# Kernel tuning notes

Measured on AMD Instinct MI355X. Metric: run time of the kernel, lower is better.

Reference implementation:

```python
import jax, jax.numpy as jnp
import numpy as np

EMBED = 1024
HEADS = 16
HEAD_DIM = EMBED // HEADS


def setup_inputs() -> dict:
    key = jax.random.key(0)
    ks = jax.random.split(key, 9)
    s = 1.0 / np.sqrt(EMBED)
    inp = {
        "x": jax.random.normal(ks[0], (2, 2048, EMBED), dtype=jnp.float32),
        "wq": jax.random.uniform(ks[1], (EMBED, EMBED), jnp.float32, -s, s),
        "bq": jax.random.uniform(ks[2], (EMBED,), jnp.float32, -s, s),
        "wk": jax.random.uniform(ks[3], (EMBED, EMBED), jnp.float32, -s, s),
        "bk": jax.random.uniform(ks[4], (EMBED,), jnp.float32, -s, s),
        "wv": jax.random.uniform(ks[5], (EMBED, EMBED), jnp.float32, -s, s),
        "bv": jax.random.uniform(ks[6], (EMBED,), jnp.float32, -s, s),
        "wo": jax.random.uniform(ks[7], (EMBED, EMBED), jnp.float32, -s, s),
        "bo": jax.random.uniform(ks[8], (EMBED,), jnp.float32, -s, s),
    }
    return inp


def reference(x, wq, bq, wk, bk, wv, bv, wo, bo):
    B, S, E = x.shape
    H, D = HEADS, HEAD_DIM
    # projections (torch Linear: y = x @ W.T + b; here weights stored as [E, E] applied as x @ W.T)
    q = (x @ wq.T + bq).reshape(B, S, H, D).transpose(0, 2, 1, 3)  # [B,H,S,D]
    k = (x @ wk.T + bk).reshape(B, S, H, D).transpose(0, 2, 1, 3)
    v = (x @ wv.T + bv).reshape(B, S, H, D).transpose(0, 2, 1, 3)
    scores = jnp.einsum("bhqd,bhkd->bhqk", q, k) / jnp.sqrt(jnp.asarray(D, x.dtype))
    attn = jax.nn.softmax(scores, axis=-1)  # dropout is identity in eval / p=0
    ctx = jnp.einsum("bhqk,bhkd->bhqd", attn, v)
    ctx = ctx.transpose(0, 2, 1, 3).reshape(B, S, E)
    return ctx @ wo.T + bo
```

## Files before the change

### kernel.cpp

```cpp
#include <hip/hip_runtime.h>
#include <hip/hip_bf16.h>

#define EMBED 1024
#define HEADS 16
#define HDIM  64
#define BATCH 2
#define SEQ   2048
#define MTOT  (BATCH*SEQ)

typedef __attribute__((ext_vector_type(8))) short bf16x8;
typedef __attribute__((ext_vector_type(4))) short bf16x4;
typedef __attribute__((ext_vector_type(4))) float f32x4;
typedef __attribute__((ext_vector_type(8))) unsigned short u16x8;
typedef __attribute__((ext_vector_type(2))) unsigned u32x2;
typedef __attribute__((ext_vector_type(4))) unsigned u32x4;

__device__ __forceinline__ unsigned pack2(float lo, float hi) {
    __hip_bfloat162 h = __float22bfloat162_rn(make_float2(lo, hi));
    unsigned u;
    __builtin_memcpy(&u, &h, sizeof(u));
    return u;
}
__device__ __forceinline__ unsigned short f2bf(float f) {
    __hip_bfloat16 h = __float2bfloat16(f);
    unsigned short u;
    __builtin_memcpy(&u, &h, sizeof(u));
    return u;
}

__device__ __forceinline__ void glds16(const void* g, void* l) {
    __builtin_amdgcn_global_load_lds(
        (const __attribute__((address_space(1))) void*)g,
        (__attribute__((address_space(3))) void*)l, 16, 0, 0);
}

__global__ __launch_bounds__(256) void preconvert(
    const float* __restrict__ x,
    const float* __restrict__ wq, const float* __restrict__ wk,
    const float* __restrict__ wv, const float* __restrict__ wo,
    unsigned short* __restrict__ xb,
    unsigned short* __restrict__ wqb, unsigned short* __restrict__ wkb,
    unsigned short* __restrict__ wvb, unsigned short* __restrict__ wob)
{
    const int NX = (MTOT * EMBED) / 4;
    const int NW = (EMBED * EMBED) / 4;
    int idx = blockIdx.x * 256 + threadIdx.x;
    const float* src;
    unsigned short* dst;
    int off;
    if (idx < NX) {
        src = x; dst = xb; off = idx;
    } else {
        int r = idx - NX;
        int w = r / NW;
        off = r - w * NW;
        src = (w == 0) ? wq : (w == 1) ? wk : (w == 2) ? wv : wo;
        dst = (w == 0) ? wqb : (w == 1) ? wkb : (w == 2) ? wvb : wob;
    }
    float4 v = ((const float4*)src)[off];
    u32x2 o;
    o[0] = pack2(v.x, v.y);
    o[1] = pack2(v.z, v.w);
    *(u32x2*)(dst + (size_t)off * 4) = o;
}

__global__ __launch_bounds__(256, 2) void qkv_proj(
    const unsigned short* __restrict__ xb,
    const unsigned short* __restrict__ wqb, const float* __restrict__ bq,
    const unsigned short* __restrict__ wkb, const float* __restrict__ bk,
    const unsigned short* __restrict__ wvb, const float* __restrict__ bv,
    unsigned short* __restrict__ qo,
    unsigned short* __restrict__ ko,
    unsigned short* __restrict__ vto)
{
    const int which = blockIdx.z;
    const unsigned short* __restrict__ w =
        (which == 0) ? wqb : (which == 1) ? wkb : wvb;
    const float* __restrict__ bias = (which == 0) ? bq : (which == 1) ? bk : bv;
    const float kscale = (which == 1) ? 0.18033688f : 1.0f;

    const int m0 = blockIdx.x * 128;
    const int n0 = blockIdx.y * 128;

    __shared__ __align__(16) unsigned short a_lds[128 * 32];
    __shared__ __align__(16) unsigned short b_lds[128 * 32];

    const int tid  = threadIdx.x;
    const int lane = tid & 63;
    const int wid  = tid >> 6;
    const int wr   = wid >> 1, wc = wid & 1;
    const int lq   = lane & 15;
    const int lg   = lane >> 4;

    f32x4 acc[4][4] = {};

    const int srow  = wid * 32 + (lane >> 2);
    const int scol8 = (lane & 3) * 8;
    const unsigned short* ap0 = xb + (size_t)(m0 + srow)      * EMBED + scol8;
    const unsigned short* ap1 = xb + (size_t)(m0 + srow + 16) * EMBED + scol8;
    const unsigned short* bp0 = w  + (size_t)(n0 + srow)      * EMBED + scol8;
    const unsigned short* bp1 = w  + (size_t)(n0 + srow + 16) * EMBED + scol8;
    unsigned short* la0 = a_lds + wid * 1024;
    unsigned short* la1 = a_lds + wid * 1024 + 512;
    unsigned short* lb0 = b_lds + wid * 1024;
    unsigned short* lb1 = b_lds + wid * 1024 + 512;

    for (int k0 = 0; k0 < EMBED; k0 += 32) {
        glds16(ap0 + k0, la0);
        glds16(ap1 + k0, la1);
        glds16(bp0 + k0, lb0);
        glds16(bp1 + k0, lb1);
        __syncthreads();
        bf16x8 af[4], bfr[4];
        #pragma unroll
        for (int i = 0; i < 4; ++i)
            af[i] = *(const bf16x8*)&a_lds[(wr*64 + i*16 + lq) * 32 + lg*8];
        #pragma unroll
        for (int j = 0; j < 4; ++j)
            bfr[j] = *(const bf16x8*)&b_lds[(wc*64 + j*16 + lq) * 32 + lg*8];
        #pragma unroll
        for (int i = 0; i < 4; ++i)
            #pragma unroll
            for (int j = 0; j < 4; ++j)
                acc[i][j] = __builtin_amdgcn_mfma_f32_16x16x32_bf16(af[i], bfr[j], acc[i][j], 0, 0, 0);
        __syncthreads();
    }

    #pragma unroll
    for (int j = 0; j < 4; ++j) {
        const int nn = n0 + wc*64 + j*16 + lq;
        const float bsv = bias[nn];
        const int h = nn >> 6, d = nn & (HDIM-1);
        #pragma unroll
        for (int i = 0; i < 4; ++i) {
            const int mmb = m0 + wr*64 + i*16 + lg*4;
            const int b = mmb >> 11;
            const int s = mmb & (SEQ-1);
            const size_t bh = (size_t)(b*HEADS + h);
            if (which == 2) {
                u32x2 ov;
                ov[0] = pack2(acc[i][j][0] + bsv, acc[i][j][1] + bsv);
                ov[1] = pack2(acc[i][j][2] + bsv, acc[i][j][3] + bsv);
                *(u32x2*)&vto[(bh*HDIM + d)*SEQ + s] = ov;
            } else {
                unsigned short* o = (which == 0) ? qo : ko;
                #pragma unroll
                for (int r = 0; r < 4; ++r)
                    o[(bh*SEQ + (s + r))*HDIM + d] = f2bf((acc[i][j][r] + bsv) * kscale);
            }
        }
    }
}

__global__ __launch_bounds__(256, 2) void attn(
    const unsigned short* __restrict__ q,
    const unsigned short* __restrict__ k,
    const unsigned short* __restrict__ vt,
    unsigned short* __restrict__ ctx)
{
    __shared__ __align__(16) unsigned char sm[2 * 16384];

    const int bid   = blockIdx.x;
    const int xcd   = bid & 7;
    const int local = bid >> 3;
    const int bh    = xcd * 4 + (local >> 4);
    const int q0    = (local & 15) * 128;
    const int b     = bh >> 4;
    const int h     = bh & (HEADS - 1);
    const int tid   = threadIdx.x;
    const int wv    = tid >> 6;
    const int lane  = tid & 63;
    const int lq = lane & 15, lg = lane >> 4;

    const unsigned short* qb = q  + (size_t)bh * SEQ * HDIM;
    const unsigned short* kb = k  + (size_t)bh * SEQ * HDIM;
    const unsigned short* vb = vt + (size_t)bh * HDIM * SEQ;

    const int lg16 = lg * 16;
    const int Sp = (((lq & 3) | (((lq >> 2) & 1) << 2)) << 4);
    const int Tp = (((lq & 3) | (((lq >> 3) & 1) << 2)) << 4);
    const int kreadA = (8*(lq >> 2) + (lq & 3)) * 128 + (lg16 ^ Sp);
    const int kreadB = kreadA ^ 64;
    const int vreadA = lq * 128 + (lg16 ^ Tp);
    const int vreadB = vreadA ^ 64;

    const int wrow = tid >> 3;
    const int c8   = tid & 7;
    const int wS   = (((wrow & 3) | (((wrow >> 3) & 1) << 2)) << 4);
    const int woff = wrow * 128 + ((c8 * 16) ^ wS);

    const int scol = c8 * 8;
    const unsigned short* kp = kb + (size_t)wrow * HDIM + scol;
    const unsigned short* vp = vb + (size_t)wrow * SEQ + scol;

    bf16x8 qf[2][2];
    #pragma unroll
    for (int t = 0; t < 2; ++t)
        #pragma unroll
        for (int hh = 0; hh < 2; ++hh)
            qf[t][hh] = *(const bf16x8*)(qb + (size_t)(q0 + wv*32 + t*16 + lq) * HDIM + hh*32 + lg*8);

    u16x8 ones_u;
    #pragma unroll
    for (int e = 0; e < 8; ++e) ones_u[e] = 0x3F80;
    const bf16x8 ones = __builtin_bit_cast(bf16x8, ones_u);

    f32x4 o[2][4] = {};
    f32x4 acc_l[2] = {};

    u16x8 kr0, kr1, vr0, vr1;

#define LOADT() do {                                                           \
    kr0 = *(const u16x8*)(kp);                                                 \
    kr1 = *(const u16x8*)(kp + 32*HDIM);                                       \
    vr0 = *(const u16x8*)(vp);                                                 \
    vr1 = *(const u16x8*)(vp + 32*SEQ);                                        \
} while (0)

#define WRITET(BF) do {                                                        \
    unsigned char* smb = sm + (BF)*16384;                                      \
    *(u16x8*)(smb +         woff) = kr0;                                       \
    *(u16x8*)(smb +  4096 + woff) = kr1;                                       \
    *(u16x8*)(smb +  8192 + woff) = vr0;                                       \
    *(u16x8*)(smb + 12288 + woff) = vr1;                                       \
} while (0)

#define COMPUTE(BF) do {                                                       \
    const unsigned char* smb = sm + (BF)*16384;                                \
    f32x4 s_[2][4];                                                            \
    _Pragma("unroll")                                                          \
    for (int sub = 0; sub < 4; ++sub) {                                        \
        const int sadd = (sub & 1) * 512 + (sub >> 1) * 4096;                  \
        bf16x8 k0 = *(const bf16x8*)(smb + sadd + kreadA);                     \
        bf16x8 k1 = *(const bf16x8*)(smb + sadd + kreadB);                     \
        _Pragma("unroll")                                                      \
        for (int t = 0; t < 2; ++t) {                                          \
            f32x4 z = {};                                                      \
            z = __builtin_amdgcn_mfma_f32_16x16x32_bf16(k0, qf[t][0], z, 0, 0, 0); \
            z = __builtin_amdgcn_mfma_f32_16x16x32_bf16(k1, qf[t][1], z, 0, 0, 0); \
            s_[t][sub] = z;                                                    \
        }                                                                      \
    }                                                                          \
    bf16x8 pb[2][2];                                                           \
    _Pragma("unroll")                                                          \
    for (int t = 0; t < 2; ++t) {                                              \
        u32x4 pw0, pw1;                                                        \
        _Pragma("unroll")                                                      \
        for (int sub = 0; sub < 4; ++sub) {                                    \
            f32x4 pv;                                                          \
            _Pragma("unroll")                                                  \
            for (int r = 0; r < 4; ++r) pv[r] = exp2f(s_[t][sub][r]);          \
            unsigned d0 = pack2(pv[0], pv[1]);                                 \
            unsigned d1 = pack2(pv[2], pv[3]);                                 \
            if (sub == 0)      { pw0[0] = d0; pw0[1] = d1; }                   \
            else if (sub == 1) { pw0[2] = d0; pw0[3] = d1; }                   \
            else if (sub == 2) { pw1[0] = d0; pw1[1] = d1; }                   \
            else               { pw1[2] = d0; pw1[3] = d1; }                   \
        }                                                                      \
        pb[t][0] = __builtin_bit_cast(bf16x8, pw0);                            \
        pb[t][1] = __builtin_bit_cast(bf16x8, pw1);                            \
        acc_l[t] = __builtin_amdgcn_mfma_f32_16x16x32_bf16(ones, pb[t][0], acc_l[t], 0, 0, 0); \
        acc_l[t] = __builtin_amdgcn_mfma_f32_16x16x32_bf16(ones, pb[t][1], acc_l[t], 0, 0, 0); \
    }                                                                          \
    _Pragma("unroll")                                                          \
    for (int i = 0; i < 4; ++i) {                                              \
        bf16x8 va  = *(const bf16x8*)(smb + 8192 + i*2048 + vreadA);           \
        bf16x8 vbq = *(const bf16x8*)(smb + 8192 + i*2048 + vreadB);           \
        _Pragma("unroll")                                                      \
        for (int t = 0; t < 2; ++t) {                                          \
            o[t][i] = __builtin_amdgcn_mfma_f32_16x16x32_bf16(va,  pb[t][0], o[t][i], 0, 0, 0); \
            o[t][i] = __builtin_amdgcn_mfma_f32_16x16x32_bf16(vbq, pb[t][1], o[t][i], 0, 0, 0); \
        }                                                                      \
    }                                                                          \
} while (0)

    LOADT();
    WRITET(0);
    __syncthreads();
    kp += 64 * HDIM;
    vp += 64;

    for (int t2 = 0; t2 < 16; ++t2) {
        {
            const int t = 2 * t2;
            if (t < 31) LOADT();
            COMPUTE(0);
            if (t < 31) {
                WRITET(1);
                __syncthreads();
                kp += 64 * HDIM;
                vp += 64;
            }
        }
        {
            const int t = 2 * t2 + 1;
            if (t < 31) LOADT();
            COMPUTE(1);
            if (t < 31) {
                WRITET(0);
                __syncthreads();
                kp += 64 * HDIM;
                vp += 64;
            }
        }
    }

#undef LOADT
#undef WRITET
#undef COMPUTE

    #pragma unroll
    for (int t = 0; t < 2; ++t) {
        const float inv = 1.0f / acc_l[t][0];
        unsigned short* cb = ctx + ((size_t)(b*SEQ + q0 + wv*32 + t*16 + lq)) * EMBED + h*HDIM;
        #pragma unroll
        for (int i = 0; i < 4; ++i) {
            u32x2 ov;
            ov[0] = pack2(o[t][i][0] * inv, o[t][i][1] * inv);
            ov[1] = pack2(o[t][i][2] * inv, o[t][i][3] * inv);
            *(u32x2*)(cb + i*16 + lg*4) = ov;
        }
    }
}

__global__ __launch_bounds__(256, 2) void out_proj(
    const unsigned short* __restrict__ ctx,
    const unsigned short* __restrict__ wob, const float* __restrict__ bo,
    float* __restrict__ out)
{
    const int m0 = blockIdx.x * 128;
    const int n0 = blockIdx.y * 128;

    __shared__ __align__(16) unsigned short a_lds[128 * 32];
    __shared__ __align__(16) unsigned short b_lds[128 * 32];

    const int tid  = threadIdx.x;
    const int lane = tid & 63;
    const int wid  = tid >> 6;
    const int wr   = wid >> 1, wc = wid & 1;
    const int lq   = lane & 15;
    const int lg   = lane >> 4;

    f32x4 acc[4][4] = {};

    const int srow  = wid * 32 + (lane >> 2);
    const int scol8 = (lane & 3) * 8;
    const unsigned short* ap0 = ctx + (size_t)(m0 + srow)      * EMBED + scol8;
    const unsigned short* ap1 = ctx + (size_t)(m0 + srow + 16) * EMBED + scol8;
    const unsigned short* bp0 = wob + (size_t)(n0 + srow)      * EMBED + scol8;
    const unsigned short* bp1 = wob + (size_t)(n0 + srow + 16) * EMBED + scol8;
    unsigned short* la0 = a_lds + wid * 1024;
    unsigned short* la1 = a_lds + wid * 1024 + 512;
    unsigned short* lb0 = b_lds + wid * 1024;
    unsigned short* lb1 = b_lds + wid * 1024 + 512;

    for (int k0 = 0; k0 < EMBED; k0 += 32) {
        glds16(ap0 + k0, la0);
        glds16(ap1 + k0, la1);
        glds16(bp0 + k0, lb0);
        glds16(bp1 + k0, lb1);
        __syncthreads();
        bf16x8 af[4], bfr[4];
        #pragma unroll
        for (int i = 0; i < 4; ++i)
            af[i] = *(const bf16x8*)&a_lds[(wr*64 + i*16 + lq) * 32 + lg*8];
        #pragma unroll
        for (int j = 0; j < 4; ++j)
            bfr[j] = *(const bf16x8*)&b_lds[(wc*64 + j*16 + lq) * 32 + lg*8];
        #pragma unroll
        for (int i = 0; i < 4; ++i)
            #pragma unroll
            for (int j = 0; j < 4; ++j)
                acc[i][j] = __builtin_amdgcn_mfma_f32_16x16x32_bf16(af[i], bfr[j], acc[i][j], 0, 0, 0);
        __syncthreads();
    }

    #pragma unroll
    for (int j = 0; j < 4; ++j) {
        const int nn = n0 + wc*64 + j*16 + lq;
        const float bsv = bo[nn];
        #pragma unroll
        for (int i = 0; i < 4; ++i) {
            const int mm = m0 + wr*64 + i*16 + lg*4;
            #pragma unroll
            for (int r = 0; r < 4; ++r)
                out[(size_t)(mm + r) * EMBED + nn] = acc[i][j][r] + bsv;
        }
    }
}

extern "C" void kernel_launch(void* const* d_in, const int* in_sizes, int n_in,
                              void* d_out, int out_size, void* d_ws, size_t ws_size,
                              hipStream_t stream) {
    const float* x  = (const float*)d_in[0];
    const float* wq = (const float*)d_in[1];
    const float* bq = (const float*)d_in[2];
    const float* wk = (const float*)d_in[3];
    const float* bk = (const float*)d_in[4];
    const float* wv = (const float*)d_in[5];
    const float* bv = (const float*)d_in[6];
    const float* wo = (const float*)d_in[7];
    const float* bo = (const float*)d_in[8];
    float* out = (float*)d_out;

    const size_t NELEM = (size_t)MTOT * EMBED;
    const size_t WELEM = (size_t)EMBED * EMBED;
    unsigned short* q_ws   = (unsigned short*)d_ws;
    unsigned short* k_ws   = q_ws  + NELEM;
    unsigned short* vt_ws  = k_ws  + NELEM;
    unsigned short* ctx_ws = vt_ws + NELEM;
    unsigned short* wqb    = ctx_ws + NELEM;
    unsigned short* wkb    = wqb + WELEM;
    unsigned short* wvb    = wkb + WELEM;
    unsigned short* wob    = wvb + WELEM;
    unsigned short* xb     = ctx_ws;

    const int NCONV = (int)((NELEM + 4 * WELEM) / 4);
    preconvert<<<dim3(NCONV / 256), 256, 0, stream>>>(
        x, wq, wk, wv, wo, xb, wqb, wkb, wvb, wob);
    qkv_proj<<<dim3(MTOT/128, EMBED/128, 3), 256, 0, stream>>>(
        xb, wqb, bq, wkb, bk, wvb, bv, q_ws, k_ws, vt_ws);
    attn<<<dim3((SEQ/128) * BATCH*HEADS), 256, 0, stream>>>(q_ws, k_ws, vt_ws, ctx_ws);
    out_proj<<<dim3(MTOT/128, EMBED/128), 256, 0, stream>>>(ctx_ws, wob, bo, out);
}
```

Baseline: 130.6 us.

## Split attention KV range across two blocks and merge partial outputs

The attention kernel is templated on a KV split count. With two splits, each block processes half of the key/value sequence and writes unnormalised fp32 partial outputs and row sums to workspace. A new merge kernel sums the partials, normalises them and writes bf16 context. This doubles the block count to fill the GPU better and raises the launch-bounds occupancy target. The cost is extra fp32 global traffic, an extra kernel launch, and possible register pressure from the tighter launch bound. The split path runs only when the workspace is large enough, and the plain sum of partials assumes the kernel does not rescale by a per-split running max.

```diff
diff --git a/kernel.cpp b/kernel.cpp
--- a/kernel.cpp
+++ b/kernel.cpp
@@ -152,19 +152,34 @@
     }
 }
 
-__global__ __launch_bounds__(256, 2) void attn(
+template<int NSPLIT>
+__global__ __launch_bounds__(256, 4) void attn(
     const unsigned short* __restrict__ q,
     const unsigned short* __restrict__ k,
     const unsigned short* __restrict__ vt,
-    unsigned short* __restrict__ ctx)
+    unsigned short* __restrict__ ctx,
+    float* __restrict__ po,
+    float* __restrict__ pl)
 {
     __shared__ __align__(16) unsigned char sm[2 * 16384];
 
     const int bid   = blockIdx.x;
     const int xcd   = bid & 7;
     const int local = bid >> 3;
-    const int bh    = xcd * 4 + (local >> 4);
-    const int q0    = (local & 15) * 128;
+    int bh, q0, split;
+    if (NSPLIT == 2) {
+        bh    = xcd * 4 + (local >> 5);
+        const int r5 = local & 31;
+        q0    = (r5 >> 1) * 128;
+        split = r5 & 1;
+    } else {
+        bh    = xcd * 4 + (local >> 4);
+        q0    = (local & 15) * 128;
+        split = 0;
+    }
+    const int kv0 = split * (SEQ / NSPLIT);
+    const int NT  = (SEQ / NSPLIT) / 64;
+
     const int b     = bh >> 4;
     const int h     = bh & (HEADS - 1);
     const int tid   = threadIdx.x;
@@ -190,8 +205,8 @@
     const int woff = wrow * 128 + ((c8 * 16) ^ wS);
 
     const int scol = c8 * 8;
-    const unsigned short* kp = kb + (size_t)wrow * HDIM + scol;
-    const unsigned short* vp = vb + (size_t)wrow * SEQ + scol;
+    const unsigned short* kp = kb + (size_t)(kv0 + wrow) * HDIM + scol;
+    const unsigned short* vp = vb + (size_t)wrow * SEQ + kv0 + scol;
 
     bf16x8 qf[2][2];
     #pragma unroll
@@ -280,12 +295,12 @@
     kp += 64 * HDIM;
     vp += 64;
 
-    for (int t2 = 0; t2 < 16; ++t2) {
+    for (int t2 = 0; t2 < NT / 2; ++t2) {
         {
             const int t = 2 * t2;
-            if (t < 31) LOADT();
+            if (t < NT - 1) LOADT();
             COMPUTE(0);
-            if (t < 31) {
+            if (t < NT - 1) {
                 WRITET(1);
                 __syncthreads();
                 kp += 64 * HDIM;
@@ -294,9 +309,9 @@
         }
         {
             const int t = 2 * t2 + 1;
-            if (t < 31) LOADT();
+            if (t < NT - 1) LOADT();
             COMPUTE(1);
-            if (t < 31) {
+            if (t < NT - 1) {
                 WRITET(0);
                 __syncthreads();
                 kp += 64 * HDIM;
@@ -309,18 +324,57 @@
 #undef WRITET
 #undef COMPUTE
 
-    #pragma unroll
-    for (int t = 0; t < 2; ++t) {
-        const float inv = 1.0f / acc_l[t][0];
-        unsigned short* cb = ctx + ((size_t)(b*SEQ + q0 + wv*32 + t*16 + lq)) * EMBED + h*HDIM;
-        #pragma unroll
-        for (int i = 0; i < 4; ++i) {
-            u32x2 ov;
-            ov[0] = pack2(o[t][i][0] * inv, o[t][i][1] * inv);
-            ov[1] = pack2(o[t][i][2] * inv, o[t][i][3] * inv);
-            *(u32x2*)(cb + i*16 + lg*4) = ov;
-        }
-    }
+    if (NSPLIT == 2) {
+        const size_t PO = (size_t)MTOT * EMBED;
+        #pragma unroll
+        for (int t = 0; t < 2; ++t) {
+            const int row = q0 + wv*32 + t*16 + lq;
+            float* pr = po + (size_t)split * PO + ((size_t)bh * SEQ + row) * HDIM;
+            #pragma unroll
+            for (int i = 0; i < 4; ++i)
+                *(f32x4*)(pr + i*16 + lg*4) = o[t][i];
+            if (lg == 0)
+                pl[(size_t)split * (32 * SEQ) + (size_t)bh * SEQ + row] = acc_l[t][0];
+        }
+    } else {
+        #pragma unroll
+        for (int t = 0; t < 2; ++t) {
+            const float inv = 1.0f / acc_l[t][0];
+            unsigned short* cb = ctx + ((size_t)(b*SEQ + q0 + wv*32 + t*16 + lq)) * EMBED + h*HDIM;
+            #pragma unroll
+            for (int i = 0; i < 4; ++i) {
+                u32x2 ov;
+                ov[0] = pack2(o[t][i][0] * inv, o[t][i][1] * inv);
+                ov[1] = pack2(o[t][i][2] * inv, o[t][i][3] * inv);
+                *(u32x2*)(cb + i*16 + lg*4) = ov;
+            }
+        }
+    }
+}
+
+__global__ __launch_bounds__(256) void merge_split(
+    const float* __restrict__ po, const float* __restrict__ pl,
+    unsigned short* __restrict__ ctx)
+{
+    const size_t PO = (size_t)MTOT * EMBED;
+    int t = blockIdx.x * 256 + threadIdx.x;
+    int e = t * 4;
+    int rh  = e >> 6;
+    int h   = rh & 15;
+    int row = rh >> 4;
+    int bInd = row >> 11;
+    int qInd = row & (SEQ - 1);
+    int bh  = bInd * HEADS + h;
+    size_t pidx = ((size_t)bh * SEQ + qInd) * HDIM + (e & 63);
+    float4 o0 = *(const float4*)(po + pidx);
+    float4 o1 = *(const float4*)(po + PO + pidx);
+    size_t lidx = (size_t)bh * SEQ + qInd;
+    float l = pl[lidx] + pl[(size_t)32 * SEQ + lidx];
+    float inv = 1.0f / l;
+    u32x2 ov;
+    ov[0] = pack2((o0.x + o1.x) * inv, (o0.y + o1.y) * inv);
+    ov[1] = pack2((o0.z + o1.z) * inv, (o0.w + o1.w) * inv);
+    *(u32x2*)(ctx + e) = ov;
 }
 
 __global__ __launch_bounds__(256, 2) void out_proj(
@@ -415,11 +469,23 @@
     unsigned short* wob    = wvb + WELEM;
     unsigned short* xb     = ctx_ws;
 
+    float* po = (float*)(wob + WELEM);
+    float* pl = po + 2 * NELEM;
+    const size_t NEED = (size_t)((char*)(pl + 2 * 32 * SEQ) - (char*)d_ws);
+    const bool use_split = ws_size >= NEED;
+
     const int NCONV = (int)((NELEM + 4 * WELEM) / 4);
     preconvert<<<dim3(NCONV / 256), 256, 0, stream>>>(
         x, wq, wk, wv, wo, xb, wqb, wkb, wvb, wob);
     qkv_proj<<<dim3(MTOT/128, EMBED/128, 3), 256, 0, stream>>>(
         xb, wqb, bq, wkb, bk, wvb, bv, q_ws, k_ws, vt_ws);
-    attn<<<dim3((SEQ/128) * BATCH*HEADS), 256, 0, stream>>>(q_ws, k_ws, vt_ws, ctx_ws);
+    if (use_split) {
+        attn<2><<<dim3((SEQ/128) * BATCH*HEADS * 2), 256, 0, stream>>>(
+            q_ws, k_ws, vt_ws, ctx_ws, po, pl);
+        merge_split<<<dim3((int)(NELEM / 4 / 256)), 256, 0, stream>>>(po, pl, ctx_ws);
+    } else {
+        attn<1><<<dim3((SEQ/128) * BATCH*HEADS), 256, 0, stream>>>(
+            q_ws, k_ws, vt_ws, ctx_ws, po, pl);
+    }
     out_proj<<<dim3(MTOT/128, EMBED/128), 256, 0, stream>>>(ctx_ws, wob, bo, out);
 }
```

Result: slower. 138.1 us (+5.8%).
